# Performance work log

Measured on AMD Instinct MI355X. Metric: run time of the kernel, lower is better.

Reference implementation:

```python
import jax, jax.numpy as jnp
import numpy as np

N_NODES = 50000
N_EDGES = 800000
D_IN = 256
D_OUT = 64
NEG_SLOPE = 0.2


def setup_inputs() -> dict:
    key = jax.random.key(0)
    k_x, k_src, k_dst, k_val, k_w = jax.random.split(key, 5)
    x = jax.random.normal(k_x, (N_NODES, D_IN), dtype=jnp.float32)
    edge_src = jax.random.randint(k_src, (N_EDGES,), 0, N_NODES, dtype=jnp.int32)
    edge_dst = jnp.sort(jax.random.randint(k_dst, (N_EDGES,), 0, N_NODES, dtype=jnp.int32))
    edge_val = jax.random.uniform(k_val, (N_EDGES,), dtype=jnp.float32)
    # xavier_uniform for Linear weight [out, in]; zeros for bias
    limit = float(np.sqrt(6.0 / (D_IN + D_OUT)))
    W = jax.random.uniform(k_w, (D_OUT, D_IN), dtype=jnp.float32, minval=-limit, maxval=limit)
    b = jnp.zeros((D_OUT,), dtype=jnp.float32)
    return {"x": x, "W": W, "b": b, "edge_src": edge_src, "edge_dst": edge_dst, "edge_val": edge_val}


def reference(x, W, b, edge_src, edge_dst, edge_val):
    # support = x @ W^T + b  -> [N, D_OUT]
    support = jnp.einsum("ni,oi->no", x, W) + b
    # sparse adj matmul: out[d] = sum_{edges e with dst=d} val[e] * support[src[e]]
    messages = edge_val[:, None] * support[edge_src]  # [E, D_OUT]
    agg = jax.ops.segment_sum(messages, edge_dst, num_segments=N_NODES)
    return jnp.where(agg >= 0, agg, NEG_SLOPE * agg)
```

## Files before the change

kernel.cpp:

```cpp
#include <hip/hip_runtime.h>

#define N_NODES 50000
#define N_EDGES 800000
#define D_IN 256
#define D_OUT 64
#define NEG_SLOPE 0.2f

#define PREP_BLOCKS 114
#define GEMM_BLOCKS 782
#define GRID1 (PREP_BLOCKS + GEMM_BLOCKS)

typedef __attribute__((ext_vector_type(8))) short bf16x8;
typedef __attribute__((ext_vector_type(4))) float f32x4;

__device__ inline ushort f2bf(float f) {
  union { float f; unsigned u; } v; v.f = f;
  unsigned r = v.u + 0x7FFFu + ((v.u >> 16) & 1u);
  return (ushort)(r >> 16);
}
__device__ inline float bf2f(ushort h) {
  union { unsigned u; float f; } v; v.u = ((unsigned)h) << 16;
  return v.f;
}

#define XLOAD(dst, off)                                                  \
  asm volatile("global_load_dwordx4 %0, %1, off offset:" #off            \
               : "=v"(dst) : "v"(xp) : "memory")

__global__ __launch_bounds__(256, 4) void gemm_prep(
    const float* __restrict__ x, const float* __restrict__ W,
    const float* __restrict__ bias,
    const int* __restrict__ edge_dst, int* __restrict__ row_ptr,
    ushort* __restrict__ support) {
  const int tid  = threadIdx.x;
  const int bid  = blockIdx.x;

  if (bid < PREP_BLOCKS) {
    for (int e = bid * 256 + tid; e < N_EDGES; e += PREP_BLOCKS * 256) {
      const int d = edge_dst[e];
      if (e == 0) {
        for (int n = 0; n <= d; ++n) row_ptr[n] = 0;
      } else {
        const int dp = edge_dst[e - 1];
        if (d != dp)
          for (int n = dp + 1; n <= d; ++n) row_ptr[n] = e;
      }
      if (e == N_EDGES - 1)
        for (int n = d + 1; n <= N_NODES; ++n) row_ptr[n] = N_EDGES;
    }
    return;
  }

  __shared__ ushort Wl[D_OUT * D_IN];
  const int wave = tid >> 6;
  const int lane = tid & 63;
  const int m0  = (bid - PREP_BLOCKS) * 64 + wave * 16;
  const int r16 = lane & 15;
  const int kg  = lane >> 4;
  int arow = m0 + r16;
  if (arow >= N_NODES) arow = N_NODES - 1;
  const float* xp = x + (size_t)arow * D_IN + kg * 8;

  f32x4 xd[16];
  XLOAD(xd[0], 0);    XLOAD(xd[1], 16);
  XLOAD(xd[2], 128);  XLOAD(xd[3], 144);
  XLOAD(xd[4], 256);  XLOAD(xd[5], 272);
  XLOAD(xd[6], 384);  XLOAD(xd[7], 400);
  XLOAD(xd[8], 512);  XLOAD(xd[9], 528);
  XLOAD(xd[10], 640); XLOAD(xd[11], 656);
  XLOAD(xd[12], 768); XLOAD(xd[13], 784);
  XLOAD(xd[14], 896); XLOAD(xd[15], 912);

  for (int c = tid; c < (D_OUT * D_IN) / 8; c += 256) {
    const int row = c >> 5;
    const int cc  = c & 31;
    const f32x4 w0 = *reinterpret_cast<const f32x4*>(W + c * 8);
    const f32x4 w1 = *reinterpret_cast<const f32x4*>(W + c * 8 + 4);
    bf16x8 v;
    v[0] = (short)f2bf(w0[0]); v[1] = (short)f2bf(w0[1]);
    v[2] = (short)f2bf(w0[2]); v[3] = (short)f2bf(w0[3]);
    v[4] = (short)f2bf(w1[0]); v[5] = (short)f2bf(w1[1]);
    v[6] = (short)f2bf(w1[2]); v[7] = (short)f2bf(w1[3]);
    unsigned byte = row * 512 + cc * 16;
    byte ^= (row & 7) << 4;
    *reinterpret_cast<bf16x8*>(reinterpret_cast<char*>(Wl) + byte) = v;
  }
  __syncthreads();

  asm volatile("s_waitcnt vmcnt(0)" ::: "memory");
  __builtin_amdgcn_sched_barrier(0);

  f32x4 acc[4] = {f32x4{0.f,0.f,0.f,0.f}, f32x4{0.f,0.f,0.f,0.f},
                  f32x4{0.f,0.f,0.f,0.f}, f32x4{0.f,0.f,0.f,0.f}};
#pragma unroll
  for (int ks = 0; ks < 8; ++ks) {
    const f32x4 xa = xd[2 * ks];
    const f32x4 xb = xd[2 * ks + 1];
    bf16x8 a;
    a[0] = (short)f2bf(xa[0]); a[1] = (short)f2bf(xa[1]);
    a[2] = (short)f2bf(xa[2]); a[3] = (short)f2bf(xa[3]);
    a[4] = (short)f2bf(xb[0]); a[5] = (short)f2bf(xb[1]);
    a[6] = (short)f2bf(xb[2]); a[7] = (short)f2bf(xb[3]);
#pragma unroll
    for (int nb = 0; nb < 4; ++nb) {
      const int row = nb * 16 + r16;
      unsigned byte = row * 512 + kg * 16 + ks * 64;
      byte ^= (row & 7) << 4;
      const bf16x8 bfrag = *reinterpret_cast<const bf16x8*>(
          reinterpret_cast<const char*>(Wl) + byte);
      acc[nb] =
          __builtin_amdgcn_mfma_f32_16x16x32_bf16(a, bfrag, acc[nb], 0, 0, 0);
    }
  }
#pragma unroll
  for (int nb = 0; nb < 4; ++nb) {
    const int col = nb * 16 + r16;
    const float bv = bias[col];
#pragma unroll
    for (int i = 0; i < 4; ++i) {
      const int row = m0 + kg * 4 + i;
      if (row < N_NODES)
        support[(size_t)row * D_OUT + col] = f2bf(acc[nb][i] + bv);
    }
  }
}

__global__ __launch_bounds__(256, 8) void agg_kernel(
    const ushort* __restrict__ support, const int* __restrict__ edge_src,
    const float* __restrict__ edge_val, const int* __restrict__ row_ptr,
    float* __restrict__ out) {
  const int wid = (blockIdx.x * 256 + threadIdx.x) >> 6;
  const int lane = threadIdx.x & 63;
  if (wid >= N_NODES) return;
  const int lo = row_ptr[wid];
  const int hi = row_ptr[wid + 1];

  float a[8];
#pragma unroll
  for (int q = 0; q < 8; ++q) a[q] = 0.f;

  int e = lo;
  for (; e + 7 < hi; e += 8) {
    int   s[8];
    float v[8];
#pragma unroll
    for (int q = 0; q < 8; ++q) { s[q] = edge_src[e + q]; v[q] = edge_val[e + q]; }
#pragma unroll
    for (int q = 0; q < 8; ++q)
      a[q] = fmaf(v[q], bf2f(support[(size_t)s[q] * D_OUT + lane]), a[q]);
  }
  if (e + 3 < hi) {
    int   s[4];
    float v[4];
#pragma unroll
    for (int q = 0; q < 4; ++q) { s[q] = edge_src[e + q]; v[q] = edge_val[e + q]; }
#pragma unroll
    for (int q = 0; q < 4; ++q)
      a[q] = fmaf(v[q], bf2f(support[(size_t)s[q] * D_OUT + lane]), a[q]);
    e += 4;
  }
  for (; e < hi; ++e)
    a[0] = fmaf(edge_val[e], bf2f(support[(size_t)edge_src[e] * D_OUT + lane]), a[0]);

  const float acc = ((a[0] + a[1]) + (a[2] + a[3])) + ((a[4] + a[5]) + (a[6] + a[7]));
  out[(size_t)wid * D_OUT + lane] = acc >= 0.f ? acc : NEG_SLOPE * acc;
}

extern "C" void kernel_launch(void* const* d_in, const int* in_sizes, int n_in,
                              void* d_out, int out_size, void* d_ws, size_t ws_size,
                              hipStream_t stream) {
  const float* x        = (const float*)d_in[0];
  const float* W        = (const float*)d_in[1];
  const float* b        = (const float*)d_in[2];
  const int*   edge_src = (const int*)d_in[3];
  const int*   edge_dst = (const int*)d_in[4];
  const float* edge_val = (const float*)d_in[5];
  float* out = (float*)d_out;

  ushort* support = (ushort*)d_ws;
  char* p = (char*)d_ws + (size_t)N_NODES * D_OUT * sizeof(ushort);
  int* row_ptr = (int*)p;

  hipLaunchKernelGGL(gemm_prep, dim3(GRID1), dim3(256), 0, stream,
                     x, W, b, edge_dst, row_ptr, support);
  hipLaunchKernelGGL(agg_kernel, dim3((N_NODES * 64 + 255) / 256), dim3(256), 0,
                     stream, support, edge_src, edge_val, row_ptr, out);
}
```

Before: 55.73 us.

## Split support into column halves and gather 8 edges per wave with vector loads

The GEMM now writes support as two 32-column bf16 halves in separate arrays. The aggregation kernel runs a 2D grid where blockIdx.y picks the half, so each half-table is smaller and more cache-resident. Within a wave, 8 edge groups of 8 lanes each load 4 bf16 values per lane (8-byte vector loads), then reduce across groups with shuffles and write float4 outputs. This cuts per-edge load instructions and raises memory-level parallelism. In exchange, edge_src and edge_val are read twice, once per half, and there is extra shuffle work.

New measurement: 58.77 us. 1.05x slower.

```diff
diff --git a/kernel.cpp b/kernel.cpp
--- a/kernel.cpp
+++ b/kernel.cpp
@@ -12,6 +12,7 @@
 
 typedef __attribute__((ext_vector_type(8))) short bf16x8;
 typedef __attribute__((ext_vector_type(4))) float f32x4;
+typedef __attribute__((ext_vector_type(4))) ushort u16x4;
 
 __device__ inline ushort f2bf(float f) {
   union { float f; unsigned u; } v; v.f = f;
@@ -31,7 +32,7 @@
     const float* __restrict__ x, const float* __restrict__ W,
     const float* __restrict__ bias,
     const int* __restrict__ edge_dst, int* __restrict__ row_ptr,
-    ushort* __restrict__ support) {
+    ushort* __restrict__ S0, ushort* __restrict__ S1) {
   const int tid  = threadIdx.x;
   const int bid  = blockIdx.x;
 
@@ -116,54 +117,65 @@
   for (int nb = 0; nb < 4; ++nb) {
     const int col = nb * 16 + r16;
     const float bv = bias[col];
+    ushort* Sh = (nb < 2) ? S0 : S1;
+    const int c2 = col & 31;
 #pragma unroll
     for (int i = 0; i < 4; ++i) {
       const int row = m0 + kg * 4 + i;
       if (row < N_NODES)
-        support[(size_t)row * D_OUT + col] = f2bf(acc[nb][i] + bv);
+        Sh[(size_t)row * 32 + c2] = f2bf(acc[nb][i] + bv);
     }
   }
 }
 
 __global__ __launch_bounds__(256, 8) void agg_kernel(
-    const ushort* __restrict__ support, const int* __restrict__ edge_src,
-    const float* __restrict__ edge_val, const int* __restrict__ row_ptr,
-    float* __restrict__ out) {
-  const int wid = (blockIdx.x * 256 + threadIdx.x) >> 6;
+    const ushort* __restrict__ S0, const ushort* __restrict__ S1,
+    const int* __restrict__ edge_src, const float* __restrict__ edge_val,
+    const int* __restrict__ row_ptr, float* __restrict__ out) {
+  const int wave = threadIdx.x >> 6;
   const int lane = threadIdx.x & 63;
-  if (wid >= N_NODES) return;
-  const int lo = row_ptr[wid];
-  const int hi = row_ptr[wid + 1];
-
-  float a[8];
-#pragma unroll
-  for (int q = 0; q < 8; ++q) a[q] = 0.f;
-
-  int e = lo;
-  for (; e + 7 < hi; e += 8) {
-    int   s[8];
-    float v[8];
-#pragma unroll
-    for (int q = 0; q < 8; ++q) { s[q] = edge_src[e + q]; v[q] = edge_val[e + q]; }
-#pragma unroll
-    for (int q = 0; q < 8; ++q)
-      a[q] = fmaf(v[q], bf2f(support[(size_t)s[q] * D_OUT + lane]), a[q]);
-  }
-  if (e + 3 < hi) {
-    int   s[4];
-    float v[4];
-#pragma unroll
-    for (int q = 0; q < 4; ++q) { s[q] = edge_src[e + q]; v[q] = edge_val[e + q]; }
-#pragma unroll
-    for (int q = 0; q < 4; ++q)
-      a[q] = fmaf(v[q], bf2f(support[(size_t)s[q] * D_OUT + lane]), a[q]);
-    e += 4;
-  }
-  for (; e < hi; ++e)
-    a[0] = fmaf(edge_val[e], bf2f(support[(size_t)edge_src[e] * D_OUT + lane]), a[0]);
-
-  const float acc = ((a[0] + a[1]) + (a[2] + a[3])) + ((a[4] + a[5]) + (a[6] + a[7]));
-  out[(size_t)wid * D_OUT + lane] = acc >= 0.f ? acc : NEG_SLOPE * acc;
+  const int node = blockIdx.x * 4 + wave;
+  if (node >= N_NODES) return;
+  const ushort* __restrict__ Sh = blockIdx.y ? S1 : S0;
+  const int lo = row_ptr[node];
+  const int hi = row_ptr[node + 1];
+  const int eg = lane >> 3;
+  const int cl = lane & 7;
+
+  f32x4 a0 = {0.f, 0.f, 0.f, 0.f};
+  f32x4 a1 = {0.f, 0.f, 0.f, 0.f};
+
+  for (int e = lo; e < hi; e += 16) {
+#pragma unroll
+    for (int q = 0; q < 2; ++q) {
+      const int idx = e + q * 8 + eg;
+      const int ic = idx < hi ? idx : hi - 1;
+      const int s  = edge_src[ic];
+      const float vv = edge_val[ic];
+      const float v = idx < hi ? vv : 0.f;
+      const u16x4 g = *reinterpret_cast<const u16x4*>(
+          Sh + (size_t)s * 32 + cl * 4);
+      f32x4& A = q ? a1 : a0;
+      A[0] = fmaf(v, bf2f(g[0]), A[0]);
+      A[1] = fmaf(v, bf2f(g[1]), A[1]);
+      A[2] = fmaf(v, bf2f(g[2]), A[2]);
+      A[3] = fmaf(v, bf2f(g[3]), A[3]);
+    }
+  }
+
+  float r[4] = {a0[0] + a1[0], a0[1] + a1[1], a0[2] + a1[2], a0[3] + a1[3]};
+#pragma unroll
+  for (int c = 0; c < 4; ++c) {
+    r[c] += __shfl_xor(r[c], 8, 64);
+    r[c] += __shfl_xor(r[c], 16, 64);
+    r[c] += __shfl_xor(r[c], 32, 64);
+    r[c] = r[c] >= 0.f ? r[c] : NEG_SLOPE * r[c];
+  }
+  if (eg == 0) {
+    f32x4 o = {r[0], r[1], r[2], r[3]};
+    *reinterpret_cast<f32x4*>(
+        out + (size_t)node * D_OUT + blockIdx.y * 32 + cl * 4) = o;
+  }
 }
 
 extern "C" void kernel_launch(void* const* d_in, const int* in_sizes, int n_in,
@@ -177,12 +189,12 @@
   const float* edge_val = (const float*)d_in[5];
   float* out = (float*)d_out;
 
-  ushort* support = (ushort*)d_ws;
-  char* p = (char*)d_ws + (size_t)N_NODES * D_OUT * sizeof(ushort);
-  int* row_ptr = (int*)p;
+  ushort* S0 = (ushort*)d_ws;
+  ushort* S1 = S0 + (size_t)N_NODES * 32;
+  int* row_ptr = (int*)(S1 + (size_t)N_NODES * 32);
 
   hipLaunchKernelGGL(gemm_prep, dim3(GRID1), dim3(256), 0, stream,
-                     x, W, b, edge_dst, row_ptr, support);
-  hipLaunchKernelGGL(agg_kernel, dim3((N_NODES * 64 + 255) / 256), dim3(256), 0,
-                     stream, support, edge_src, edge_val, row_ptr, out);
-}
+                     x, W, b, edge_dst, row_ptr, S0, S1);
+  hipLaunchKernelGGL(agg_kernel, dim3((N_NODES + 3) / 4, 2), dim3(256), 0,
+                     stream, S0, S1, edge_src, edge_val, row_ptr, out);
+}
```
